# Kernel optimization log

Measured on AMD Instinct MI355X. Metric: run time of the kernel, lower is better.

The kernel has to match this reference:

```python
import jax, jax.numpy as jnp
import numpy as np

EPS = 1e-8  # torch cosine_similarity eps

def _cnorm(x):
    return jnp.maximum(jnp.linalg.norm(x, axis=-1), EPS)

def setup_inputs() -> dict:
    key = jax.random.key(0)
    ks = jax.random.split(key, 9)
    B, K, dp, Ms = 16384, 16, 64, 32
    content = jax.random.normal(ks[0], (B, K, dp), jnp.float32)
    types = jax.random.uniform(ks[1], (B, K, 3), jnp.float32)
    conf = jax.random.uniform(ks[2], (B, K), jnp.float32)
    S = jax.random.normal(ks[3], (B, Ms, dp), jnp.float32)
    s1 = 1.0 / np.sqrt(dp)   # torch Linear init bound, fan_in=dp
    s2 = 1.0 / np.sqrt(2 * dp)  # fan_in=2*dp
    W_ante = jax.random.uniform(ks[4], (dp, dp), jnp.float32, -s1, s1)
    W_cons = jax.random.uniform(ks[5], (dp, 2 * dp), jnp.float32, -s2, s2)
    W_gamma_w = jax.random.uniform(ks[6], (dp, 2 * dp), jnp.float32, -s2, s2)
    W_gamma_b = jnp.zeros((dp,), jnp.float32)
    log_fire_threshold = jnp.asarray(np.log(0.5), jnp.float32)
    return {"content": content, "types": types, "conf": conf, "S": S,
            "W_ante": W_ante, "W_cons": W_cons, "W_gamma_w": W_gamma_w,
            "W_gamma_b": W_gamma_b, "log_fire_threshold": log_fire_threshold}

def reference(content, types, conf, S, W_ante, W_cons, W_gamma_w, W_gamma_b, log_fire_threshold):
    # InferenceEngine.forward_chain, vectorized over rules and batch.
    B, K, dp = content.shape
    p_fact = types[..., 0]  # FACT channel
    p_rule = types[..., 1]  # RULE channel
    thr = jnp.exp(log_fire_threshold)

    ante = content @ W_ante.T                                   # [B,K,dp]
    dots = jnp.einsum('bkd,bjd->bkj', ante, content)            # [B,K_rule,K_fact]
    sim = dots / (_cnorm(ante)[:, :, None] * _cnorm(content)[:, None, :])
    match_scores = sim * p_fact[:, None, :]
    match_strength = jnp.einsum('bkj,bj->bk', match_scores, conf)
    fire = jax.nn.sigmoid((match_strength - thr) / 0.5) * p_rule  # [B,K]
    matched = jnp.einsum('bkj,bjd->bkd', match_scores, content)
    new_fact = jnp.concatenate([content, matched], -1) @ W_cons.T  # [B,K,dp]
    derived_conf = fire * conf                                     # [B,K]

    def soft_write(S, cand, dconf):
        # batched LatentScratchpad.soft_write; cand [B,dp], dconf [B]
        dot = jnp.einsum('bd,bmd->bm', cand, S)
        s = dot / (_cnorm(cand)[:, None] * _cnorm(S))
        alpha = jax.nn.softmax(s * 4.0, axis=-1)                  # [B,Ms]
        best = jnp.argmax(alpha, axis=-1)
        best_slots = jnp.take_along_axis(S, best[:, None, None], axis=1)[:, 0, :]
        gamma = jax.nn.sigmoid(jnp.concatenate([best_slots, cand], -1) @ W_gamma_w.T + W_gamma_b)
        new_content = gamma * cand + (1.0 - gamma) * best_slots
        return S + dconf[:, None, None] * alpha[..., None] * (new_content[:, None, :] - S)

    def step(S, xs):
        nf_k, fire_k, dc_k = xs
        S_w = soft_write(S, nf_k, dc_k)
        mask = (fire_k > 0.1)[:, None, None]  # replaces per-element .item() branch
        return jnp.where(mask, S_w, S), None

    xs = (jnp.swapaxes(new_fact, 0, 1), fire.T, derived_conf.T)   # scan over K rules (sequential dep on S)
    S_new, _ = jax.lax.scan(step, S, xs)
    best_derived_conf = jnp.max(derived_conf, axis=-1)
    return S_new, best_derived_conf
```

## Files before the change

### kernel.cpp

```cpp
#include <hip/hip_runtime.h>
#include <math.h>

typedef float v2f __attribute__((ext_vector_type(2)));
typedef float v4f __attribute__((ext_vector_type(4)));
typedef short bs8 __attribute__((ext_vector_type(8)));

__device__ __forceinline__ float hsum(v2f a) { return a.x + a.y; }
__device__ __forceinline__ float rsq_(float x) { return __builtin_amdgcn_rsqf(fmaxf(x, 1e-16f)); }
__device__ __forceinline__ float rcp_(float x) { return __builtin_amdgcn_rcpf(x); }

__device__ __forceinline__ void pk4(v2f& acc, v4f a, v4f b) {
    acc += a.xy * b.xy;
    acc += a.zw * b.zw;
}

__device__ __forceinline__ short bf16rne_(float x) {
    unsigned u = __float_as_uint(x);
    return (short)((u + 0x7FFFu + ((u >> 16) & 1)) >> 16);
}

template<int CTRL>
__device__ __forceinline__ float dpp_add_(float x) {
    int r = __builtin_amdgcn_update_dpp(0, __float_as_int(x), CTRL, 0xF, 0xF, true);
    return x + __int_as_float(r);
}
template<int CTRL>
__device__ __forceinline__ float dpp_max_(float x) {
    int r = __builtin_amdgcn_update_dpp(__float_as_int(x), __float_as_int(x), CTRL, 0xF, 0xF, false);
    return fmaxf(x, __int_as_float(r));
}
__device__ __forceinline__ float dpp_sum64(float x) {
    x = dpp_add_<0x111>(x);
    x = dpp_add_<0x112>(x);
    x = dpp_add_<0x114>(x);
    x = dpp_add_<0x118>(x);
    x = dpp_add_<0x142>(x);
    x = dpp_add_<0x143>(x);
    return __int_as_float(__builtin_amdgcn_readlane(__float_as_int(x), 63));
}
__device__ __forceinline__ float dpp_max64(float x) {
    x = dpp_max_<0x111>(x);
    x = dpp_max_<0x112>(x);
    x = dpp_max_<0x114>(x);
    x = dpp_max_<0x118>(x);
    x = dpp_max_<0x142>(x);
    x = dpp_max_<0x143>(x);
    return __int_as_float(__builtin_amdgcn_readlane(__float_as_int(x), 63));
}

__global__ __launch_bounds__(256, 2)
void dense_kernel(const float* __restrict__ content,
                  const float* __restrict__ types,
                  const float* __restrict__ conf,
                  const float* __restrict__ W_ante,
                  const float* __restrict__ W_cons,
                  const float* __restrict__ lft,
                  float* __restrict__ out, int B)
{
    const int tid = threadIdx.x;
    const int l = tid & 63;
    const int w = tid >> 6;
    const int b = blockIdx.x * 4 + w;

    __shared__ float s_cont[4][16*68];
    __shared__ float s_scr [4][16*68];
    __shared__ float s_ms  [4][16*20];
    __shared__ float s_sm  [4][96];
    __shared__ bs8   s_bA[512];
    __shared__ bs8   s_b1[512];
    __shared__ bs8   s_b2[512];

    #pragma unroll
    for (int it = 0; it < 6; it++) {
        const int fid = tid + it*256;
        const int mat = fid >> 9, rem = fid & 511;
        const int fl  = rem & 63;
        const int row = ((rem >> 7) & 3)*16 + (fl & 15);
        const int kb  = ((rem >> 6) & 1)*32 + (fl >> 4)*8;
        const float* src = (mat == 0) ? (W_ante + row*64 + kb)
                                      : (W_cons + row*128 + kb + ((mat == 2) ? 64 : 0));
        bs8 v;
        #pragma unroll
        for (int e = 0; e < 8; e++) v[e] = bf16rne_(src[e]);
        bs8* dst = (mat == 0) ? s_bA : (mat == 1) ? s_b1 : s_b2;
        dst[rem] = v;
    }
    __syncthreads();
    if (b >= B) return;

    float* cont = s_cont[w];
    float* scr  = s_scr[w];
    float* ms   = s_ms[w];
    float* sm   = s_sm[w];

    const float thr = expf(lft[0]);

    float c[16];
    const float* cb = content + ((size_t)b << 10);
    #pragma unroll
    for (int k = 0; k < 16; k++) {
        float v = cb[(k << 6) + l];
        c[k] = v;
        cont[k*68 + l] = v;
    }
    if (l < 16) {
        sm[0  + l] = conf[((size_t)b << 4) + l];
        sm[16 + l] = types[(((size_t)b << 4) + l)*3 + 0];
        sm[32 + l] = types[(((size_t)b << 4) + l)*3 + 1];
    }

    {
        const int k = l & 15, q = l >> 4;
        const v4f* row = (const v4f*)&cont[k*68 + q*16];
        v2f s2 = {0.f, 0.f};
        #pragma unroll
        for (int i = 0; i < 4; i++) { v4f v = row[i]; pk4(s2, v, v); }
        float s = hsum(s2);
        s += __shfl_xor(s, 16, 64);
        s += __shfl_xor(s, 32, 64);
        if (l < 16) sm[48 + l] = rsq_(s);
    }

    bs8 aC[2];
    #pragma unroll
    for (int s = 0; s < 2; s++) {
        const float* ap = &cont[(l & 15)*68 + s*32 + (l >> 4)*8];
        v4f p0 = *(const v4f*)ap;
        v4f p1 = *(const v4f*)(ap + 4);
        bs8 v;
        v[0]=bf16rne_(p0.x); v[1]=bf16rne_(p0.y); v[2]=bf16rne_(p0.z); v[3]=bf16rne_(p0.w);
        v[4]=bf16rne_(p1.x); v[5]=bf16rne_(p1.y); v[6]=bf16rne_(p1.z); v[7]=bf16rne_(p1.w);
        aC[s] = v;
    }

    #pragma unroll
    for (int t = 0; t < 4; t++) {
        v4f acc = {0.f, 0.f, 0.f, 0.f};
        acc = __builtin_amdgcn_mfma_f32_16x16x32_bf16(aC[0], s_bA[(t*2+0)*64 + l], acc, 0, 0, 0);
        acc = __builtin_amdgcn_mfma_f32_16x16x32_bf16(aC[1], s_bA[(t*2+1)*64 + l], acc, 0, 0, 0);
        #pragma unroll
        for (int r = 0; r < 4; r++)
            scr[((l >> 4)*4 + r)*68 + t*16 + (l & 15)] = acc[r];
    }

    {
        const int k = l & 15, q = l >> 4;
        const v4f* row = (const v4f*)&scr[k*68 + q*16];
        v2f s2 = {0.f, 0.f};
        #pragma unroll
        for (int i = 0; i < 4; i++) { v4f v = row[i]; pk4(s2, v, v); }
        float s = hsum(s2);
        s += __shfl_xor(s, 16, 64);
        s += __shfl_xor(s, 32, 64);
        if (l < 16) sm[64 + l] = rsq_(s);
    }

    {
        const int k = l & 15, jg4 = (l >> 4) * 4;
        const v4f* ar = (const v4f*)&scr[k*68];
        const v4f* c0 = (const v4f*)&cont[(jg4+0)*68];
        const v4f* c1 = (const v4f*)&cont[(jg4+1)*68];
        const v4f* c2 = (const v4f*)&cont[(jg4+2)*68];
        const v4f* c3 = (const v4f*)&cont[(jg4+3)*68];
        v2f d0 = {0,0}, d1 = {0,0}, d2 = {0,0}, d3 = {0,0};
        #pragma unroll
        for (int i = 0; i < 16; i++) {
            v4f a = ar[i];
            v4f x0 = c0[i]; d0 += a.xy*x0.xy; d0 += a.zw*x0.zw;
            v4f x1 = c1[i]; d1 += a.xy*x1.xy; d1 += a.zw*x1.zw;
            v4f x2 = c2[i]; d2 += a.xy*x2.xy; d2 += a.zw*x2.zw;
            v4f x3 = c3[i]; d3 += a.xy*x3.xy; d3 += a.zw*x3.zw;
        }
        const float ra = sm[64 + k];
        v4f res;
        res.x = hsum(d0) * ra * sm[48 + jg4+0] * sm[16 + jg4+0];
        res.y = hsum(d1) * ra * sm[48 + jg4+1] * sm[16 + jg4+1];
        res.z = hsum(d2) * ra * sm[48 + jg4+2] * sm[16 + jg4+2];
        res.w = hsum(d3) * ra * sm[48 + jg4+3] * sm[16 + jg4+3];
        *(v4f*)&ms[k*20 + jg4] = res;
    }

    float dc_l = 0.f;
    if (l < 16) {
        const v4f* mr = (const v4f*)&ms[l*20];
        const v4f* cf = (const v4f*)&sm[0];
        v2f st = {0.f, 0.f};
        #pragma unroll
        for (int i = 0; i < 4; i++) { v4f m4 = mr[i]; v4f f4 = cf[i]; st += m4.xy*f4.xy; st += m4.zw*f4.zw; }
        float str = hsum(st);
        float fire = sm[32 + l] * rcp_(1.0f + __expf(-(str - thr) * 2.0f));
        float dcf  = fire * sm[0 + l];
        out[((size_t)b << 11) + 1024 + l] = fire;
        out[((size_t)b << 11) + 1040 + l] = dcf;
        dc_l = dcf;
    }
    {
        float mv = dc_l;
        mv = fmaxf(mv, __shfl_xor(mv, 1, 64));
        mv = fmaxf(mv, __shfl_xor(mv, 2, 64));
        mv = fmaxf(mv, __shfl_xor(mv, 4, 64));
        mv = fmaxf(mv, __shfl_xor(mv, 8, 64));
        if (l == 0) out[((size_t)B << 11) + b] = mv;
    }

    float mt[16];
    #pragma unroll
    for (int k = 0; k < 16; k++) {
        const v4f* mr = (const v4f*)&ms[k*20];
        v2f m2 = {0.f, 0.f};
        #pragma unroll
        for (int i = 0; i < 4; i++) {
            v4f m4 = mr[i];
            v2f clo = {c[4*i+0], c[4*i+1]};
            v2f chi = {c[4*i+2], c[4*i+3]};
            m2 += m4.xy*clo; m2 += m4.zw*chi;
        }
        mt[k] = hsum(m2);
    }
    #pragma unroll
    for (int k = 0; k < 16; k++) scr[k*68 + l] = mt[k];

    bs8 aM[2];
    #pragma unroll
    for (int s = 0; s < 2; s++) {
        const float* ap = &scr[(l & 15)*68 + s*32 + (l >> 4)*8];
        v4f p0 = *(const v4f*)ap;
        v4f p1 = *(const v4f*)(ap + 4);
        bs8 v;
        v[0]=bf16rne_(p0.x); v[1]=bf16rne_(p0.y); v[2]=bf16rne_(p0.z); v[3]=bf16rne_(p0.w);
        v[4]=bf16rne_(p1.x); v[5]=bf16rne_(p1.y); v[6]=bf16rne_(p1.z); v[7]=bf16rne_(p1.w);
        aM[s] = v;
    }

    v4f nfacc[4];
    #pragma unroll
    for (int t = 0; t < 4; t++) {
        v4f acc = {0.f, 0.f, 0.f, 0.f};
        acc = __builtin_amdgcn_mfma_f32_16x16x32_bf16(aC[0], s_b1[(t*2+0)*64 + l], acc, 0, 0, 0);
        acc = __builtin_amdgcn_mfma_f32_16x16x32_bf16(aC[1], s_b1[(t*2+1)*64 + l], acc, 0, 0, 0);
        acc = __builtin_amdgcn_mfma_f32_16x16x32_bf16(aM[0], s_b2[(t*2+0)*64 + l], acc, 0, 0, 0);
        acc = __builtin_amdgcn_mfma_f32_16x16x32_bf16(aM[1], s_b2[(t*2+1)*64 + l], acc, 0, 0, 0);
        nfacc[t] = acc;
    }

    #pragma unroll
    for (int t = 0; t < 4; t++) {
        #pragma unroll
        for (int r = 0; r < 4; r++) {
            out[((size_t)b << 11) + (size_t)(((l >> 4)*4 + r) << 6) + t*16 + (l & 15)] = nfacc[t][r];
        }
    }

    #pragma unroll
    for (int r = 0; r < 4; r++) {
        float s = 0.f;
        #pragma unroll
        for (int t = 0; t < 4; t++) s += nfacc[t][r]*nfacc[t][r];
        s += __shfl_xor(s, 1, 64);
        s += __shfl_xor(s, 2, 64);
        s += __shfl_xor(s, 4, 64);
        s += __shfl_xor(s, 8, 64);
        if ((l & 15) == 0)
            out[((size_t)b << 11) + 1056 + (l >> 4)*4 + r] = rsq_(s);
    }
}

__global__ __launch_bounds__(512, 4)
void scan_kernel(const float* __restrict__ Sg,
                 const float* __restrict__ W_gw,
                 const float* __restrict__ W_gb,
                 float* __restrict__ out, int B)
{
    const int t = threadIdx.x;
    const int l = t & 63;
    const int w = t >> 6;
    const int b = (blockIdx.x << 3) + w;

    __shared__ v4f            w1v[1024];
    __shared__ float          snf_  [8][16*64];
    __shared__ unsigned short gcB_  [8][16*64];
    __shared__ float          smeta_[8][48];
    __shared__ float          bsb_  [8][68];
    __shared__ float          ncb_  [8][68];
    float* snf   = snf_[w];
    unsigned short* gcB = gcB_[w];
    float* smeta = smeta_[w];
    float* bsb   = bsb_[w];
    float* ncb   = ncb_[w];

    const int m = l & 31, h = l >> 5;

    {
        #pragma unroll
        for (int j = 0; j < 2; j++) {
            const int i = (w << 1) + j;
            w1v[i*64 + l] = *(const v4f*)&W_gw[(size_t)l*128 + i*4];
        }
    }

    v2f Sreg[16];

    if (b < B) {
        if (l < 48) smeta[l] = out[((size_t)b << 11) + 1024 + l];

        const float* nfb = out + ((size_t)b << 11);
        #pragma unroll
        for (int i = 0; i < 4; i++) {
            *(v4f*)&snf[i*256 + l*4] = *(const v4f*)&nfb[i*256 + l*4];
        }

        {
            const float* srow = Sg + ((size_t)b << 11) + (m << 6) + (h << 5);
            #pragma unroll
            for (int i = 0; i < 8; i++) {
                v4f v = *(const v4f*)&srow[i*4];
                Sreg[2*i]   = v.xy;
                Sreg[2*i+1] = v.zw;
            }
        }

        {
            v2f wB[32];
            const v4f* w2 = (const v4f*)(W_gw + ((size_t)l << 7) + 64);
            #pragma unroll
            for (int i = 0; i < 16; i++) { v4f v = w2[i]; wB[2*i] = v.xy; wB[2*i+1] = v.zw; }
            #pragma unroll
            for (int k = 0; k < 16; k++) {
                const v4f* cr = (const v4f*)&snf[k << 6];
                v2f a = {0.f, 0.f};
                #pragma unroll
                for (int i = 0; i < 16; i++) { v4f v = cr[i]; a += v.xy*wB[2*i]; a += v.zw*wB[2*i+1]; }
                const float g = hsum(a);
                gcB[(k << 6) + l] = (unsigned short)((__float_as_uint(g) + 0x8000u) >> 16);
            }
        }
    }

    __syncthreads();
    if (b >= B) return;

    const float gb = W_gb[l];

    #pragma unroll 1
    for (int k = 0; k < 16; k++) {
        const float fire = smeta[k];
        if (fire <= 0.1f) continue;
        const float dck  = smeta[16 + k];
        const float rncn = smeta[32 + k];
        const float gck  = __uint_as_float((unsigned)gcB[(k << 6) + l] << 16);
        const float cd   = snf[(k << 6) + l];

        v2f d2 = {0.f, 0.f}, n2 = {0.f, 0.f};
        {
            const v4f* cr = (const v4f*)&snf[(k << 6) + (h << 5)];
            #pragma unroll
            for (int i = 0; i < 8; i++) {
                v4f c = cr[i];
                d2 += Sreg[2*i]*c.xy;       d2 += Sreg[2*i+1]*c.zw;
                n2 += Sreg[2*i]*Sreg[2*i];  n2 += Sreg[2*i+1]*Sreg[2*i+1];
            }
        }
        float dt = hsum(d2);
        float nn = hsum(n2);
        dt += __shfl_xor(dt, 32, 64);
        nn += __shfl_xor(nn, 32, 64);
        const float sc = dt * rsq_(nn) * rncn;
        const float e  = __expf(4.0f * sc);

        const float mx = dpp_max64(sc);
        const unsigned long long bal = __ballot(sc == mx);
        const int best = __ffsll(bal & 0xffffffffULL) - 1;

        if (m == best) {
            #pragma unroll
            for (int j = 0; j < 8; j++) {
                v4f v = { Sreg[2*j].x, Sreg[2*j].y, Sreg[2*j+1].x, Sreg[2*j+1].y };
                *(v4f*)&bsb[(h << 5) + j*4] = v;
            }
        }

        const float tot = dpp_sum64(e);
        const float wm  = dck * e * 2.0f * rcp_(tot);

        v2f g2 = {0.f, 0.f};
        {
            const v4f* wrow = &w1v[l];
            #pragma unroll
            for (int i = 0; i < 16; i++) {
                v4f bs = *(const v4f*)&bsb[i*4];
                v4f wv = wrow[i*64];
                g2 += bs.xy*wv.xy; g2 += bs.zw*wv.zw;
            }
        }
        const float g = gb + gck + hsum(g2);
        const float gamma = rcp_(1.0f + __expf(-g));
        const float bsd = bsb[l];
        ncb[l] = gamma*cd + (1.0f - gamma)*bsd;

        const v2f wm2 = {wm, wm};
        {
            const v4f* nr = (const v4f*)&ncb[h << 5];
            #pragma unroll
            for (int i = 0; i < 8; i++) {
                v4f nc = nr[i];
                Sreg[2*i]   += wm2 * (nc.xy - Sreg[2*i]);
                Sreg[2*i+1] += wm2 * (nc.zw - Sreg[2*i+1]);
            }
        }
    }

    {
        float* ob = out + ((size_t)b << 11) + (m << 6) + (h << 5);
        #pragma unroll
        for (int j = 0; j < 8; j++) {
            v4f v = { Sreg[2*j].x, Sreg[2*j].y, Sreg[2*j+1].x, Sreg[2*j+1].y };
            *(v4f*)&ob[j*4] = v;
        }
    }
}

extern "C" void kernel_launch(void* const* d_in, const int* in_sizes, int n_in,
                              void* d_out, int out_size, void* d_ws, size_t ws_size,
                              hipStream_t stream) {
    const float* content = (const float*)d_in[0];
    const float* types   = (const float*)d_in[1];
    const float* conf    = (const float*)d_in[2];
    const float* S       = (const float*)d_in[3];
    const float* W_ante  = (const float*)d_in[4];
    const float* W_cons  = (const float*)d_in[5];
    const float* W_gw    = (const float*)d_in[6];
    const float* W_gb    = (const float*)d_in[7];
    const float* lft     = (const float*)d_in[8];

    const int B = in_sizes[0] / 1024;

    hipLaunchKernelGGL(dense_kernel, dim3((B + 3) / 4), dim3(256), 0, stream,
                       content, types, conf, W_ante, W_cons, lft, (float*)d_out, B);
    hipLaunchKernelGGL(scan_kernel, dim3((B + 7) / 8), dim3(512), 0, stream,
                       S, W_gw, W_gb, (float*)d_out, B);
}
```

Baseline: 237.7 us.

## Move gamma candidate projection into dense kernel via MFMA, store as bf16

The per-rule gamma contribution from the candidate (new_fact @ W_gamma_w[:,64:]) is now computed in the dense kernel with bf16 MFMA instead of scalar FP32 loops in the scan kernel. The result goes to the output buffer as bf16 in scratch space, and the scan reads it per step from global memory. The scan kernel also keeps the slot-half of W_gamma_w in LDS as bf16 to halve LDS use, and reuses bsb in place of ncb. This moves scan-kernel prologue work onto matrix cores and lowers LDS pressure, at the cost of extra global traffic and a global load inside the sequential loop.

Result: faster. 216.8 us (-8.8%).

```diff
diff --git a/kernel.cpp b/kernel.cpp
--- a/kernel.cpp
+++ b/kernel.cpp
@@ -17,6 +17,9 @@
 __device__ __forceinline__ short bf16rne_(float x) {
     unsigned u = __float_as_uint(x);
     return (short)((u + 0x7FFFu + ((u >> 16) & 1)) >> 16);
+}
+__device__ __forceinline__ float bf2f_(short s) {
+    return __uint_as_float((unsigned)(unsigned short)s << 16);
 }
 
 template<int CTRL>
@@ -54,6 +57,7 @@
                   const float* __restrict__ conf,
                   const float* __restrict__ W_ante,
                   const float* __restrict__ W_cons,
+                  const float* __restrict__ W_gw,
                   const float* __restrict__ lft,
                   float* __restrict__ out, int B)
 {
@@ -69,20 +73,23 @@
     __shared__ bs8   s_bA[512];
     __shared__ bs8   s_b1[512];
     __shared__ bs8   s_b2[512];
-
-    #pragma unroll
-    for (int it = 0; it < 6; it++) {
+    __shared__ bs8   s_bG[512];
+
+    #pragma unroll
+    for (int it = 0; it < 8; it++) {
         const int fid = tid + it*256;
         const int mat = fid >> 9, rem = fid & 511;
         const int fl  = rem & 63;
         const int row = ((rem >> 7) & 3)*16 + (fl & 15);
         const int kb  = ((rem >> 6) & 1)*32 + (fl >> 4)*8;
         const float* src = (mat == 0) ? (W_ante + row*64 + kb)
-                                      : (W_cons + row*128 + kb + ((mat == 2) ? 64 : 0));
+                         : (mat == 1) ? (W_cons + row*128 + kb)
+                         : (mat == 2) ? (W_cons + row*128 + 64 + kb)
+                         :              (W_gw  + row*128 + 64 + kb);
         bs8 v;
         #pragma unroll
         for (int e = 0; e < 8; e++) v[e] = bf16rne_(src[e]);
-        bs8* dst = (mat == 0) ? s_bA : (mat == 1) ? s_b1 : s_b2;
+        bs8* dst = (mat == 0) ? s_bA : (mat == 1) ? s_b1 : (mat == 2) ? s_b2 : s_bG;
         dst[rem] = v;
     }
     __syncthreads();
@@ -247,7 +254,9 @@
     for (int t = 0; t < 4; t++) {
         #pragma unroll
         for (int r = 0; r < 4; r++) {
-            out[((size_t)b << 11) + (size_t)(((l >> 4)*4 + r) << 6) + t*16 + (l & 15)] = nfacc[t][r];
+            const int krow = (l >> 4)*4 + r, dcol = t*16 + (l & 15);
+            scr[krow*68 + dcol] = nfacc[t][r];
+            out[((size_t)b << 11) + (size_t)(krow << 6) + dcol] = nfacc[t][r];
         }
     }
 
@@ -262,6 +271,29 @@
         s += __shfl_xor(s, 8, 64);
         if ((l & 15) == 0)
             out[((size_t)b << 11) + 1056 + (l >> 4)*4 + r] = rsq_(s);
+    }
+
+    bs8 aN[2];
+    #pragma unroll
+    for (int s = 0; s < 2; s++) {
+        const float* ap = &scr[(l & 15)*68 + s*32 + (l >> 4)*8];
+        v4f p0 = *(const v4f*)ap;
+        v4f p1 = *(const v4f*)(ap + 4);
+        bs8 v;
+        v[0]=bf16rne_(p0.x); v[1]=bf16rne_(p0.y); v[2]=bf16rne_(p0.z); v[3]=bf16rne_(p0.w);
+        v[4]=bf16rne_(p1.x); v[5]=bf16rne_(p1.y); v[6]=bf16rne_(p1.z); v[7]=bf16rne_(p1.w);
+        aN[s] = v;
+    }
+
+    unsigned short* gco = (unsigned short*)(out + ((size_t)b << 11) + 1088);
+    #pragma unroll
+    for (int t = 0; t < 4; t++) {
+        v4f acc = {0.f, 0.f, 0.f, 0.f};
+        acc = __builtin_amdgcn_mfma_f32_16x16x32_bf16(aN[0], s_bG[(t*2+0)*64 + l], acc, 0, 0, 0);
+        acc = __builtin_amdgcn_mfma_f32_16x16x32_bf16(aN[1], s_bG[(t*2+1)*64 + l], acc, 0, 0, 0);
+        #pragma unroll
+        for (int r = 0; r < 4; r++)
+            gco[(((l >> 4)*4 + r) << 6) + t*16 + (l & 15)] = (unsigned short)bf16rne_(acc[r]);
     }
 }
 
@@ -276,26 +308,22 @@
     const int w = t >> 6;
     const int b = (blockIdx.x << 3) + w;
 
-    __shared__ v4f            w1v[1024];
-    __shared__ float          snf_  [8][16*64];
-    __shared__ unsigned short gcB_  [8][16*64];
-    __shared__ float          smeta_[8][48];
-    __shared__ float          bsb_  [8][68];
-    __shared__ float          ncb_  [8][68];
+    __shared__ bs8   w1b[512];
+    __shared__ float snf_  [8][16*64];
+    __shared__ float smeta_[8][48];
+    __shared__ float bsb_  [8][68];
     float* snf   = snf_[w];
-    unsigned short* gcB = gcB_[w];
     float* smeta = smeta_[w];
     float* bsb   = bsb_[w];
-    float* ncb   = ncb_[w];
 
     const int m = l & 31, h = l >> 5;
 
     {
-        #pragma unroll
-        for (int j = 0; j < 2; j++) {
-            const int i = (w << 1) + j;
-            w1v[i*64 + l] = *(const v4f*)&W_gw[(size_t)l*128 + i*4];
-        }
+        const float* src = W_gw + (size_t)(t & 63)*128 + (t >> 6)*8;
+        bs8 v;
+        #pragma unroll
+        for (int e = 0; e < 8; e++) v[e] = bf16rne_(src[e]);
+        w1b[(t >> 6)*64 + (t & 63)] = v;
     }
 
     v2f Sreg[16];
@@ -309,36 +337,19 @@
             *(v4f*)&snf[i*256 + l*4] = *(const v4f*)&nfb[i*256 + l*4];
         }
 
-        {
-            const float* srow = Sg + ((size_t)b << 11) + (m << 6) + (h << 5);
-            #pragma unroll
-            for (int i = 0; i < 8; i++) {
-                v4f v = *(const v4f*)&srow[i*4];
-                Sreg[2*i]   = v.xy;
-                Sreg[2*i+1] = v.zw;
-            }
-        }
-
-        {
-            v2f wB[32];
-            const v4f* w2 = (const v4f*)(W_gw + ((size_t)l << 7) + 64);
-            #pragma unroll
-            for (int i = 0; i < 16; i++) { v4f v = w2[i]; wB[2*i] = v.xy; wB[2*i+1] = v.zw; }
-            #pragma unroll
-            for (int k = 0; k < 16; k++) {
-                const v4f* cr = (const v4f*)&snf[k << 6];
-                v2f a = {0.f, 0.f};
-                #pragma unroll
-                for (int i = 0; i < 16; i++) { v4f v = cr[i]; a += v.xy*wB[2*i]; a += v.zw*wB[2*i+1]; }
-                const float g = hsum(a);
-                gcB[(k << 6) + l] = (unsigned short)((__float_as_uint(g) + 0x8000u) >> 16);
-            }
+        const float* srow = Sg + ((size_t)b << 11) + (m << 6) + (h << 5);
+        #pragma unroll
+        for (int i = 0; i < 8; i++) {
+            v4f v = *(const v4f*)&srow[i*4];
+            Sreg[2*i]   = v.xy;
+            Sreg[2*i+1] = v.zw;
         }
     }
 
     __syncthreads();
     if (b >= B) return;
 
+    const unsigned short* gcg = (const unsigned short*)(out + ((size_t)b << 11) + 1088);
     const float gb = W_gb[l];
 
     #pragma unroll 1
@@ -347,7 +358,7 @@
         if (fire <= 0.1f) continue;
         const float dck  = smeta[16 + k];
         const float rncn = smeta[32 + k];
-        const float gck  = __uint_as_float((unsigned)gcB[(k << 6) + l] << 16);
+        const unsigned short gcu = gcg[(k << 6) + l];
         const float cd   = snf[(k << 6) + l];
 
         v2f d2 = {0.f, 0.f}, n2 = {0.f, 0.f};
@@ -384,22 +395,29 @@
 
         v2f g2 = {0.f, 0.f};
         {
-            const v4f* wrow = &w1v[l];
+            const bs8* wrow = &w1b[l];
             #pragma unroll
-            for (int i = 0; i < 16; i++) {
-                v4f bs = *(const v4f*)&bsb[i*4];
-                v4f wv = wrow[i*64];
-                g2 += bs.xy*wv.xy; g2 += bs.zw*wv.zw;
+            for (int i = 0; i < 8; i++) {
+                bs8 w8 = wrow[i*64];
+                v4f bs0 = *(const v4f*)&bsb[i*8];
+                v4f bs1 = *(const v4f*)&bsb[i*8 + 4];
+                v2f w01 = {bf2f_(w8[0]), bf2f_(w8[1])};
+                v2f w23 = {bf2f_(w8[2]), bf2f_(w8[3])};
+                v2f w45 = {bf2f_(w8[4]), bf2f_(w8[5])};
+                v2f w67 = {bf2f_(w8[6]), bf2f_(w8[7])};
+                g2 += bs0.xy*w01; g2 += bs0.zw*w23;
+                g2 += bs1.xy*w45; g2 += bs1.zw*w67;
             }
         }
+        const float gck = bf2f_((short)gcu);
         const float g = gb + gck + hsum(g2);
         const float gamma = rcp_(1.0f + __expf(-g));
         const float bsd = bsb[l];
-        ncb[l] = gamma*cd + (1.0f - gamma)*bsd;
+        bsb[l] = gamma*cd + (1.0f - gamma)*bsd;
 
         const v2f wm2 = {wm, wm};
         {
-            const v4f* nr = (const v4f*)&ncb[h << 5];
+            const v4f* nr = (const v4f*)&bsb[h << 5];
             #pragma unroll
             for (int i = 0; i < 8; i++) {
                 v4f nc = nr[i];
@@ -435,7 +453,7 @@
     const int B = in_sizes[0] / 1024;
 
     hipLaunchKernelGGL(dense_kernel, dim3((B + 3) / 4), dim3(256), 0, stream,
-                       content, types, conf, W_ante, W_cons, lft, (float*)d_out, B);
+                       content, types, conf, W_ante, W_cons, W_gw, lft, (float*)d_out, B);
     hipLaunchKernelGGL(scan_kernel, dim3((B + 7) / 8), dim3(512), 0, stream,
                        S, W_gw, W_gb, (float*)d_out, B);
 }
```
